# Optimization experiments

Measured on AMD Instinct MI355X. Metric: run time of the kernel, lower is better.

The kernel has to match this reference:

```python
import jax, jax.numpy as jnp
import numpy as np

N, E, C_IN, HID, K, NLAYERS = 1024, 2048, 4, 192, 5, 4


def setup_inputs() -> dict:
    key = jax.random.key(0)
    ks = jax.random.split(key, 24)
    s = 0.05
    x = jax.random.normal(ks[0], (N, C_IN), jnp.float32)
    src = jax.random.randint(ks[1], (E,), 0, N, dtype=jnp.int32)
    off = jax.random.randint(ks[2], (E,), 1, N, dtype=jnp.int32)
    dst = (src + off) % N  # guarantees no self-loops (ChebConv removes them)
    edge_index = jnp.stack([src, dst])  # [2, E] int32
    edge_attr = jax.random.normal(ks[3], (E, C_IN), jnp.float32)
    batch = jnp.zeros((N,), jnp.int32)  # unused by forward, kept for signature fidelity
    inp = {
        'x': x, 'edge_index': edge_index, 'edge_attr': edge_attr, 'batch': batch,
        # ChebConv(4, 192, K=5): K weight mats + bias
        'cheb_w': jax.random.normal(ks[4], (K, C_IN, HID), jnp.float32) * s,
        'cheb_b': jnp.zeros((HID,), jnp.float32),
        # edge encoder Linear(4, 192)
        'eenc_w': jax.random.normal(ks[5], (C_IN, HID), jnp.float32) * s,
        'eenc_b': jnp.zeros((HID,), jnp.float32),
        # 4 NNConv layers, each with MapE2NxN edge MLP (192->192->192*192),
        # root linear (192x192, no bias) and conv bias
        'nn1_w': jax.random.normal(ks[6], (NLAYERS, HID, HID), jnp.float32) * s,
        'nn1_b': jnp.zeros((NLAYERS, HID), jnp.float32),
        'nn2_w': jax.random.normal(ks[7], (NLAYERS, HID, HID * HID), jnp.float32) * (s / 8.0),
        'nn2_b': jnp.zeros((NLAYERS, HID * HID), jnp.float32),
        'root_w': jax.random.normal(ks[8], (NLAYERS, HID, HID), jnp.float32) * s,
        'conv_b': jnp.zeros((NLAYERS, HID), jnp.float32),
        # LayerNorm per DeepGCNLayer
        'ln_g': jnp.ones((NLAYERS, HID), jnp.float32),
        'ln_b': jnp.zeros((NLAYERS, HID), jnp.float32),
        # final Linear(192, 2)
        'out_w': jax.random.normal(ks[9], (HID, 2), jnp.float32) * s,
        'out_b': jnp.zeros((2,), jnp.float32),
    }
    return inp


def _layernorm(v, g, b):
    mu = jnp.mean(v, axis=-1, keepdims=True)
    var = jnp.mean(jnp.square(v - mu), axis=-1, keepdims=True)
    return (v - mu) * jax.lax.rsqrt(var + 1e-5) * g + b


def reference(x, edge_index, edge_attr, batch, cheb_w, cheb_b, eenc_w, eenc_b,
              nn1_w, nn1_b, nn2_w, nn2_b, root_w, conv_b, ln_g, ln_b, out_w, out_b):
    n = x.shape[0]
    src, dst = edge_index[0], edge_index[1]

    # ---- ChebConv (sym norm, lambda_max=2.0) => L_hat = -D^{-1/2} A D^{-1/2} ----
    deg = jax.ops.segment_sum(jnp.ones_like(src, dtype=x.dtype), src, num_segments=n)
    dinv = jnp.where(deg > 0, 1.0 / jnp.sqrt(jnp.maximum(deg, 1.0)), 0.0)
    wnorm = -dinv[src] * dinv[dst]  # [E]

    def lap(v):  # y = L_hat @ v : gather -> weight -> scatter-add
        return jax.ops.segment_sum(wnorm[:, None] * v[src], dst, num_segments=n)

    Tx0 = x
    out = Tx0 @ cheb_w[0]
    Tx1 = lap(Tx0)
    out = out + Tx1 @ cheb_w[1]
    for k in range(2, K):  # Chebyshev recurrence
        Tx2 = 2.0 * lap(Tx1) - Tx0
        out = out + Tx2 @ cheb_w[k]
        Tx0, Tx1 = Tx1, Tx2
    h = out + cheb_b  # [N, HID]

    # ---- edge encoder ----
    ea = edge_attr @ eenc_w + eenc_b  # [E, HID]

    # ---- NNConv: per-edge MLP-generated weight, gather->edge-GEMM->scatter ----
    def nnconv(v, i):
        theta = (ea @ nn1_w[i] + nn1_b[i]) @ nn2_w[i] + nn2_b[i]  # [E, HID*HID]
        theta = theta.reshape(E, HID, HID)
        msg = jnp.einsum('ei,eio->eo', v[src], theta)  # per-edge matvec
        agg = jax.ops.segment_sum(msg, dst, num_segments=n)  # aggr='add'
        return agg + v @ root_w[i] + conv_b[i]

    # layers[0].conv applied directly (no pre-norm/act)
    h = nnconv(h, 0)
    # layers[1:4] are DeepGCNLayer res+: x + conv(dropout(act(norm(x))))
    for i in range(1, NLAYERS):
        z = jax.nn.relu(_layernorm(h, ln_g[i], ln_b[i]))
        h = h + nnconv(z, i)
    # final: act(layers[0].norm(x)), dropout (eval=identity), linear
    h = jax.nn.relu(_layernorm(h, ln_g[0], ln_b[0]))
    return h @ out_w + out_b  # [N, 2]
```

## Files before the change

kernel.cpp:

```cpp
#include <hip/hip_runtime.h>
#include <stdint.h>

typedef _Float16 half8 __attribute__((ext_vector_type(8)));
typedef float f32x4 __attribute__((ext_vector_type(4)));

__global__ __launch_bounds__(256)
void k_pb(const float* __restrict__ nn2_w, const float* __restrict__ eenc_w,
          const float* __restrict__ eenc_b, const float* __restrict__ nn1_w,
          const float* __restrict__ nn1_b, float* __restrict__ Ppart,
          const float* __restrict__ x, const int* __restrict__ ei,
          float* __restrict__ Tx, int* __restrict__ rowptr, int* __restrict__ eord) {
  __shared__ __align__(16) float smem[8192];
  int t = threadIdx.x;
  if (blockIdx.x == 144) {
    if (blockIdx.y == 0 && blockIdx.z == 0) {
      float* cur = smem;
      float* yv = smem + 4096;
      float* deg = yv;
      for (int i = t; i < 1024; i += 256) deg[i] = 0.f;
      __syncthreads();
      for (int e = t; e < 2048; e += 256) atomicAdd(&deg[ei[e]], 1.f);
      __syncthreads();
      float wn[8];
#pragma unroll
      for (int i = 0; i < 8; ++i) {
        int e = t + 256 * i;
        int s = ei[e], d = ei[2048 + e];
        float ds = deg[s], dd = deg[d];
        float a = ds > 0.f ? 1.f / sqrtf(fmaxf(ds, 1.f)) : 0.f;
        float b = dd > 0.f ? 1.f / sqrtf(fmaxf(dd, 1.f)) : 0.f;
        wn[i] = -a * b;
      }
      __syncthreads();
      float4 prev[4];
#pragma unroll
      for (int q = 0; q < 4; ++q) {
        int i = t + 256 * q;
        float4 xv = ((const float4*)x)[i];
        ((float4*)cur)[i] = xv;
        ((float4*)Tx)[i] = xv;
      }
      __syncthreads();
      for (int rec = 0; rec < 4; ++rec) {
        for (int i = t; i < 4096; i += 256) yv[i] = 0.f;
        __syncthreads();
#pragma unroll
        for (int i = 0; i < 8; ++i) {
          int e = t + 256 * i;
          int s = ei[e], d = ei[2048 + e];
          float wv = wn[i];
#pragma unroll
          for (int c = 0; c < 4; ++c) atomicAdd(&yv[d * 4 + c], wv * cur[s * 4 + c]);
        }
        __syncthreads();
        float a = rec ? 2.f : 1.f;
#pragma unroll
        for (int q = 0; q < 4; ++q) {
          int i = t + 256 * q;
          float4 y4 = ((float4*)yv)[i];
          float4 c4 = ((float4*)cur)[i];
          float4 n4;
          n4.x = a * y4.x - (rec ? prev[q].x : 0.f);
          n4.y = a * y4.y - (rec ? prev[q].y : 0.f);
          n4.z = a * y4.z - (rec ? prev[q].z : 0.f);
          n4.w = a * y4.w - (rec ? prev[q].w : 0.f);
          prev[q] = c4;
          ((float4*)cur)[i] = n4;
          ((float4*)(Tx + (rec + 1) * 4096))[i] = n4;
        }
        __syncthreads();
      }
    } else if (blockIdx.y == 1 && blockIdx.z == 0) {
      int* cnt = (int*)smem;
      int* rp  = (int*)smem + 1024;
      int* wtot = (int*)smem + 2048;
      int lane = t & 63, wv = t >> 6;
      for (int i = t; i < 1024; i += 256) cnt[i] = 0;
      __syncthreads();
      for (int e = t; e < 2048; e += 256) atomicAdd(&cnt[ei[2048 + e]], 1);
      __syncthreads();
      int c0 = cnt[t * 4], c1 = cnt[t * 4 + 1], c2 = cnt[t * 4 + 2], c3 = cnt[t * 4 + 3];
      int s = c0 + c1 + c2 + c3;
      int inc = s;
#pragma unroll
      for (int off = 1; off < 64; off <<= 1) {
        int u = __shfl_up(inc, off);
        if (lane >= off) inc += u;
      }
      if (lane == 63) wtot[wv] = inc;
      __syncthreads();
      int woff = 0;
#pragma unroll
      for (int j = 0; j < 4; ++j) if (j < wv) woff += wtot[j];
      int excl = woff + inc - s;
      int4 r4; r4.x = excl; r4.y = excl + c0; r4.z = excl + c0 + c1; r4.w = excl + c0 + c1 + c2;
      *(int4*)(rowptr + t * 4) = r4;
      if (t == 0) rowptr[1024] = 2048;
      rp[t * 4] = r4.x; rp[t * 4 + 1] = r4.y; rp[t * 4 + 2] = r4.z; rp[t * 4 + 3] = r4.w;
      __syncthreads();
      for (int e = t; e < 2048; e += 256) {
        int d = ei[2048 + e];
        int slot = atomicAdd(&rp[d], 1);
        eord[slot] = e;
      }
    }
    return;
  }
  int l = blockIdx.y, kc = blockIdx.z;
  if (t < 192) {
    float a0 = 0.f, a1 = 0.f, a2 = 0.f, a3 = 0.f, a4 = 0.f;
    const float* nw = nn1_w + (size_t)l * 36864 + t;
    for (int k = 0; k < 192; ++k) {
      float nv = nw[(size_t)k * 192];
      a0 += eenc_w[k] * nv;
      a1 += eenc_w[192 + k] * nv;
      a2 += eenc_w[384 + k] * nv;
      a3 += eenc_w[576 + k] * nv;
      a4 += eenc_b[k] * nv;
    }
    smem[t] = a0; smem[192 + t] = a1; smem[384 + t] = a2; smem[576 + t] = a3;
    smem[768 + t] = a4 + nn1_b[l * 192 + t];
  }
  __syncthreads();
  int col = blockIdx.x * 256 + t;
  const float* Wp = nn2_w + (size_t)l * 7077888 + (size_t)(kc * 96) * 36864 + col;
  const float* Mp = smem + kc * 96;
  float a0 = 0.f, a1 = 0.f, a2 = 0.f, a3 = 0.f, a4 = 0.f;
#pragma unroll 8
  for (int k = 0; k < 96; ++k) {
    float wv = Wp[(size_t)k * 36864];
    a0 += wv * Mp[k];
    a1 += wv * Mp[192 + k];
    a2 += wv * Mp[384 + k];
    a3 += wv * Mp[576 + k];
    a4 += wv * Mp[768 + k];
  }
  float* Pp = Ppart + ((size_t)(kc * 4 + l) * 5) * 36864 + col;
  Pp[0] = a0;
  Pp[36864] = a1;
  Pp[2 * 36864] = a2;
  Pp[3 * 36864] = a3;
  Pp[4 * 36864] = a4;
}

__global__ __launch_bounds__(256)
void k_stage(const float* __restrict__ Ppart, const float* __restrict__ nn2_b,
             const float* __restrict__ root_w, _Float16* __restrict__ Btl,
             const float* __restrict__ Tx, const float* __restrict__ cheb_w,
             const float* __restrict__ cheb_b, _Float16* __restrict__ z0) {
  int t = threadIdx.x;
  if (blockIdx.y < 4) {
    int ck = blockIdx.x, l = blockIdx.y;
    _Float16* out = Btl + (size_t)l * 221184 + ck * 9216;
#pragma unroll
    for (int it = 0; it < 5; ++it) {
      int n = it * 256 + t;
      if (n >= 1152) break;
      union { _Float16 h[8]; uint4 v; } u;
      if (n < 960) {
        int c = n / 192, o = n - c * 192;
        const float* P0 = Ppart + ((size_t)(0 * 4 + l) * 5 + c) * 36864;
        const float* P1 = Ppart + ((size_t)(1 * 4 + l) * 5 + c) * 36864;
#pragma unroll
        for (int j = 0; j < 8; ++j) {
          int io = (ck * 8 + j) * 192 + o;
          float val = P0[io] + P1[io];
          if (c == 4) val += nn2_b[(size_t)l * 36864 + io];
          u.h[j] = (_Float16)val;
        }
      } else {
        int o = n - 960;
#pragma unroll
        for (int j = 0; j < 8; ++j)
          u.h[j] = (_Float16)root_w[(size_t)l * 36864 + (ck * 8 + j) * 192 + o];
      }
      *(uint4*)(out + (size_t)n * 8) = u.v;
    }
  } else {
    for (int i = blockIdx.x * 256 + t; i < 24576; i += 6144) {
      int n = i & 1023, ck = i >> 10;
      float tv[5][4];
#pragma unroll
      for (int k = 0; k < 5; ++k) {
        float4 t4 = ((const float4*)(Tx + k * 4096))[n];
        tv[k][0] = t4.x; tv[k][1] = t4.y; tv[k][2] = t4.z; tv[k][3] = t4.w;
      }
      union { _Float16 h[8]; uint4 v; } u;
#pragma unroll
      for (int j = 0; j < 8; ++j) {
        int o = ck * 8 + j;
        float acc = cheb_b[o];
#pragma unroll
        for (int k = 0; k < 5; ++k)
#pragma unroll
          for (int c = 0; c < 4; ++c)
            acc += tv[k][c] * cheb_w[(k * 4 + c) * 192 + o];
        u.h[j] = (_Float16)acc;
      }
      *(uint4*)(z0 + ((size_t)ck * 1024 + n) * 8) = u.v;
    }
  }
}

__global__ __launch_bounds__(256)
void k_y(const _Float16* __restrict__ z16, const _Float16* __restrict__ Btl,
         float* __restrict__ Y, int layer) {
  int t = threadIdx.x;
  int w = t >> 6, lane = t & 63, l15 = lane & 15, q4 = lane >> 4;
  int e0 = blockIdx.x * 64, cb = blockIdx.y;
  const _Float16* Bt = Btl + (size_t)layer * 221184;
  const _Float16* ap = z16 + (((size_t)q4 * 1024) + e0 + w * 16 + l15) * 8;
  const _Float16* bp = Bt + (((size_t)q4 * 1152) + cb * 192 + l15) * 8;
  f32x4 acc[12] = {};
#pragma unroll
  for (int ks = 0; ks < 6; ++ks) {
    half8 av = *(const half8*)(ap + (size_t)ks * 4 * 1024 * 8);
#pragma unroll
    for (int nt = 0; nt < 12; ++nt) {
      half8 bv = *(const half8*)(bp + (size_t)ks * 4 * 1152 * 8 + nt * 16 * 8);
      acc[nt] = __builtin_amdgcn_mfma_f32_16x16x32_f16(av, bv, acc[nt], 0, 0, 0);
    }
  }
#pragma unroll
  for (int nt = 0; nt < 12; ++nt) {
    int col = cb * 192 + nt * 16 + l15;
#pragma unroll
    for (int r = 0; r < 4; ++r) {
      int row = e0 + w * 16 + q4 * 4 + r;
      Y[(size_t)row * 1152 + col] = acc[nt][r];
    }
  }
}

__global__ __launch_bounds__(256)
void k_gn(const int* __restrict__ ei, const float* __restrict__ eattr,
          const int* __restrict__ rowptr, const int* __restrict__ eord,
          const float* __restrict__ Y, const float* __restrict__ hp,
          const float* __restrict__ cbv, const float* __restrict__ gg,
          const float* __restrict__ bb, float* __restrict__ ho,
          _Float16* __restrict__ zo, const float* __restrict__ out_w,
          const float* __restrict__ out_b, float* __restrict__ outp, int l) {
  int t = threadIdx.x, w = t >> 6, lane = t & 63;
  int n = blockIdx.x * 4 + w;
  int o0 = lane, o1 = lane + 64, o2 = lane + 128;
  float v0 = 0.f, v1 = 0.f, v2 = 0.f;
  int beg = rowptr[n], end = rowptr[n + 1];
  for (int idx = beg; idx < end; ++idx) {
    int e = eord[idx];
    int s = ei[e];
    float4 u = ((const float4*)eattr)[e];
    const float* yr = Y + (size_t)s * 1152;
    v0 += yr[o0] * u.x + yr[192 + o0] * u.y + yr[384 + o0] * u.z + yr[576 + o0] * u.w + yr[768 + o0];
    v1 += yr[o1] * u.x + yr[192 + o1] * u.y + yr[384 + o1] * u.z + yr[576 + o1] * u.w + yr[768 + o1];
    v2 += yr[o2] * u.x + yr[192 + o2] * u.y + yr[384 + o2] * u.z + yr[576 + o2] * u.w + yr[768 + o2];
  }
  const float* yn = Y + (size_t)n * 1152 + 960;
  v0 += yn[o0] + cbv[o0]; v1 += yn[o1] + cbv[o1]; v2 += yn[o2] + cbv[o2];
  if (l > 0) {
    v0 += hp[n * 192 + o0]; v1 += hp[n * 192 + o1]; v2 += hp[n * 192 + o2];
  }
  if (l < 3) {
    ho[n * 192 + o0] = v0; ho[n * 192 + o1] = v1; ho[n * 192 + o2] = v2;
  }
  float s1 = v0 + v1 + v2, s2 = v0 * v0 + v1 * v1 + v2 * v2;
#pragma unroll
  for (int off = 32; off >= 1; off >>= 1) {
    s1 += __shfl_xor(s1, off);
    s2 += __shfl_xor(s2, off);
  }
  float mu = s1 * (1.f / 192.f);
  float var = s2 * (1.f / 192.f) - mu * mu;
  float rcp = rsqrtf(var + 1e-5f);
  float z0v = fmaxf((v0 - mu) * rcp * gg[o0] + bb[o0], 0.f);
  float z1v = fmaxf((v1 - mu) * rcp * gg[o1] + bb[o1], 0.f);
  float z2v = fmaxf((v2 - mu) * rcp * gg[o2] + bb[o2], 0.f);
  if (l < 3) {
    zo[((size_t)(o0 >> 3) * 1024 + n) * 8 + (o0 & 7)] = (_Float16)z0v;
    zo[((size_t)(o1 >> 3) * 1024 + n) * 8 + (o1 & 7)] = (_Float16)z1v;
    zo[((size_t)(o2 >> 3) * 1024 + n) * 8 + (o2 & 7)] = (_Float16)z2v;
  } else {
    float a0 = z0v * out_w[o0 * 2] + z1v * out_w[o1 * 2] + z2v * out_w[o2 * 2];
    float a1 = z0v * out_w[o0 * 2 + 1] + z1v * out_w[o1 * 2 + 1] + z2v * out_w[o2 * 2 + 1];
#pragma unroll
    for (int off = 32; off >= 1; off >>= 1) {
      a0 += __shfl_xor(a0, off);
      a1 += __shfl_xor(a1, off);
    }
    if (lane == 0) {
      outp[n * 2] = a0 + out_b[0];
      outp[n * 2 + 1] = a1 + out_b[1];
    }
  }
}

extern "C" void kernel_launch(void* const* d_in, const int* in_sizes, int n_in,
                              void* d_out, int out_size, void* d_ws, size_t ws_size,
                              hipStream_t stream) {
  const float* x      = (const float*)d_in[0];
  const int*   ei     = (const int*)  d_in[1];
  const float* eattr  = (const float*)d_in[2];
  const float* cheb_w = (const float*)d_in[4];
  const float* cheb_b = (const float*)d_in[5];
  const float* eenc_w = (const float*)d_in[6];
  const float* eenc_b = (const float*)d_in[7];
  const float* nn1_w  = (const float*)d_in[8];
  const float* nn1_b  = (const float*)d_in[9];
  const float* nn2_w  = (const float*)d_in[10];
  const float* nn2_b  = (const float*)d_in[11];
  const float* root_w = (const float*)d_in[12];
  const float* conv_b = (const float*)d_in[13];
  const float* ln_g   = (const float*)d_in[14];
  const float* ln_bb  = (const float*)d_in[15];
  const float* out_w  = (const float*)d_in[16];
  const float* out_b  = (const float*)d_in[17];
  float* outp = (float*)d_out;
  (void)in_sizes; (void)n_in; (void)out_size; (void)ws_size;

  char* p = (char*)d_ws;
  _Float16* Btl = (_Float16*)p; p += (size_t)4 * 221184 * 2;
  float* Ppart  = (float*)p;    p += (size_t)2 * 4 * 5 * 36864 * 4;
  float* Tx     = (float*)p;    p += 5 * 4096 * 4;
  float* Y      = (float*)p;    p += (size_t)1024 * 1152 * 4;
  float* hA     = (float*)p;    p += 196608 * 4;
  float* hB     = (float*)p;    p += 196608 * 4;
  _Float16* z0  = (_Float16*)p; p += 196608 * 2;
  _Float16* zA  = (_Float16*)p; p += 196608 * 2;
  _Float16* zB  = (_Float16*)p; p += 196608 * 2;
  int* rowptr   = (int*)p;      p += 1056 * 4;
  int* eord     = (int*)p;      p += 2048 * 4;

  k_pb<<<dim3(145, 4, 2), 256, 0, stream>>>(nn2_w, eenc_w, eenc_b, nn1_w, nn1_b,
                                            Ppart, x, ei, Tx, rowptr, eord);
  k_stage<<<dim3(24, 5), 256, 0, stream>>>(Ppart, nn2_b, root_w, Btl, Tx,
                                           cheb_w, cheb_b, z0);

  const _Float16* zin[4] = {z0, zA, zB, zA};
  _Float16* zout[4] = {zA, zB, zA, zA};
  float* hout[4] = {hA, hB, hA, hA};
  const float* hres[4] = {hA, hA, hB, hA};
  for (int l = 0; l < 4; ++l) {
    k_y<<<dim3(16, 6), 256, 0, stream>>>(zin[l], Btl, Y, l);
    k_gn<<<256, 256, 0, stream>>>(ei, eattr, rowptr, eord, Y, hres[l],
                                  conv_b + (size_t)l * 192,
                                  ln_g + (size_t)((l == 3) ? 0 : (l + 1)) * 192,
                                  ln_bb + (size_t)((l == 3) ? 0 : (l + 1)) * 192,
                                  hout[l], zout[l], out_w, out_b, outp, l);
  }
}
```

Baseline: 299.6 us.

## Split precompute into separate kernel and double-buffer nn2_w streaming via LDS

Moves the per-layer M computation (eenc through nn1), the Chebyshev recurrence and the CSR build out of k_pb into a small k_pre kernel, so the big nn2_w reduction blocks no longer each recompute M. k_pb now handles 512 columns per block, streams 8-row tiles of nn2_w into LDS with global_load_lds in a double-buffered loop, and gives each thread two columns. The aim is better memory-level parallelism on the roughly 113 MB weight read and removal of redundant M work. The cost is an extra kernel launch and a serial dependency on k_pre, whose single Chebyshev block now runs before k_pb instead of alongside it.

Measured after the change: 321.4 us. 7.3% more time.

```diff
diff --git a/kernel.cpp b/kernel.cpp
--- a/kernel.cpp
+++ b/kernel.cpp
@@ -4,143 +4,189 @@
 typedef _Float16 half8 __attribute__((ext_vector_type(8)));
 typedef float f32x4 __attribute__((ext_vector_type(4)));
 
-__global__ __launch_bounds__(256)
-void k_pb(const float* __restrict__ nn2_w, const float* __restrict__ eenc_w,
-          const float* __restrict__ eenc_b, const float* __restrict__ nn1_w,
-          const float* __restrict__ nn1_b, float* __restrict__ Ppart,
-          const float* __restrict__ x, const int* __restrict__ ei,
-          float* __restrict__ Tx, int* __restrict__ rowptr, int* __restrict__ eord) {
+typedef const __attribute__((address_space(1))) void* gptr_t;
+typedef __attribute__((address_space(3))) void* lptr_t;
+static __device__ __forceinline__ void gll16(const void* g, void* l) {
+  __builtin_amdgcn_global_load_lds((gptr_t)(unsigned long long)g,
+                                   (lptr_t)(unsigned int)(unsigned long long)l,
+                                   16, 0, 0);
+}
+
+__global__ __launch_bounds__(256)
+void k_pre(const float* __restrict__ eenc_w, const float* __restrict__ eenc_b,
+           const float* __restrict__ nn1_w, const float* __restrict__ nn1_b,
+           const float* __restrict__ x, const int* __restrict__ ei,
+           float* __restrict__ Mbuf, float* __restrict__ Tx,
+           int* __restrict__ rowptr, int* __restrict__ eord) {
   __shared__ __align__(16) float smem[8192];
   int t = threadIdx.x;
-  if (blockIdx.x == 144) {
-    if (blockIdx.y == 0 && blockIdx.z == 0) {
-      float* cur = smem;
-      float* yv = smem + 4096;
-      float* deg = yv;
-      for (int i = t; i < 1024; i += 256) deg[i] = 0.f;
+  int b = blockIdx.x;
+  if (b < 4) {
+    int l = b;
+    if (t < 192) {
+      float a0 = 0.f, a1 = 0.f, a2 = 0.f, a3 = 0.f, a4 = 0.f;
+      const float* nw = nn1_w + (size_t)l * 36864 + t;
+      for (int k = 0; k < 192; ++k) {
+        float nv = nw[(size_t)k * 192];
+        a0 += eenc_w[k] * nv;
+        a1 += eenc_w[192 + k] * nv;
+        a2 += eenc_w[384 + k] * nv;
+        a3 += eenc_w[576 + k] * nv;
+        a4 += eenc_b[k] * nv;
+      }
+      float* Ml = Mbuf + l * 960;
+      Ml[t] = a0; Ml[192 + t] = a1; Ml[384 + t] = a2; Ml[576 + t] = a3;
+      Ml[768 + t] = a4 + nn1_b[l * 192 + t];
+    }
+  } else if (b == 4) {
+    float* cur = smem;
+    float* yv = smem + 4096;
+    float* deg = yv;
+    for (int i = t; i < 1024; i += 256) deg[i] = 0.f;
+    __syncthreads();
+    for (int e = t; e < 2048; e += 256) atomicAdd(&deg[ei[e]], 1.f);
+    __syncthreads();
+    float wn[8];
+#pragma unroll
+    for (int i = 0; i < 8; ++i) {
+      int e = t + 256 * i;
+      int s = ei[e], d = ei[2048 + e];
+      float ds = deg[s], dd = deg[d];
+      float a = ds > 0.f ? 1.f / sqrtf(fmaxf(ds, 1.f)) : 0.f;
+      float bb = dd > 0.f ? 1.f / sqrtf(fmaxf(dd, 1.f)) : 0.f;
+      wn[i] = -a * bb;
+    }
+    __syncthreads();
+    float4 prev[4];
+#pragma unroll
+    for (int q = 0; q < 4; ++q) {
+      int i = t + 256 * q;
+      float4 xv = ((const float4*)x)[i];
+      ((float4*)cur)[i] = xv;
+      ((float4*)Tx)[i] = xv;
+    }
+    __syncthreads();
+    for (int rec = 0; rec < 4; ++rec) {
+      for (int i = t; i < 4096; i += 256) yv[i] = 0.f;
       __syncthreads();
-      for (int e = t; e < 2048; e += 256) atomicAdd(&deg[ei[e]], 1.f);
-      __syncthreads();
-      float wn[8];
 #pragma unroll
       for (int i = 0; i < 8; ++i) {
         int e = t + 256 * i;
         int s = ei[e], d = ei[2048 + e];
-        float ds = deg[s], dd = deg[d];
-        float a = ds > 0.f ? 1.f / sqrtf(fmaxf(ds, 1.f)) : 0.f;
-        float b = dd > 0.f ? 1.f / sqrtf(fmaxf(dd, 1.f)) : 0.f;
-        wn[i] = -a * b;
+        float wv = wn[i];
+#pragma unroll
+        for (int c = 0; c < 4; ++c) atomicAdd(&yv[d * 4 + c], wv * cur[s * 4 + c]);
       }
       __syncthreads();
-      float4 prev[4];
+      float a = rec ? 2.f : 1.f;
 #pragma unroll
       for (int q = 0; q < 4; ++q) {
         int i = t + 256 * q;
-        float4 xv = ((const float4*)x)[i];
-        ((float4*)cur)[i] = xv;
-        ((float4*)Tx)[i] = xv;
+        float4 y4 = ((float4*)yv)[i];
+        float4 c4 = ((float4*)cur)[i];
+        float4 n4;
+        n4.x = a * y4.x - (rec ? prev[q].x : 0.f);
+        n4.y = a * y4.y - (rec ? prev[q].y : 0.f);
+        n4.z = a * y4.z - (rec ? prev[q].z : 0.f);
+        n4.w = a * y4.w - (rec ? prev[q].w : 0.f);
+        prev[q] = c4;
+        ((float4*)cur)[i] = n4;
+        ((float4*)(Tx + (rec + 1) * 4096))[i] = n4;
       }
       __syncthreads();
-      for (int rec = 0; rec < 4; ++rec) {
-        for (int i = t; i < 4096; i += 256) yv[i] = 0.f;
-        __syncthreads();
-#pragma unroll
-        for (int i = 0; i < 8; ++i) {
-          int e = t + 256 * i;
-          int s = ei[e], d = ei[2048 + e];
-          float wv = wn[i];
-#pragma unroll
-          for (int c = 0; c < 4; ++c) atomicAdd(&yv[d * 4 + c], wv * cur[s * 4 + c]);
-        }
-        __syncthreads();
-        float a = rec ? 2.f : 1.f;
-#pragma unroll
-        for (int q = 0; q < 4; ++q) {
-          int i = t + 256 * q;
-          float4 y4 = ((float4*)yv)[i];
-          float4 c4 = ((float4*)cur)[i];
-          float4 n4;
-          n4.x = a * y4.x - (rec ? prev[q].x : 0.f);
-          n4.y = a * y4.y - (rec ? prev[q].y : 0.f);
-          n4.z = a * y4.z - (rec ? prev[q].z : 0.f);
-          n4.w = a * y4.w - (rec ? prev[q].w : 0.f);
-          prev[q] = c4;
-          ((float4*)cur)[i] = n4;
-          ((float4*)(Tx + (rec + 1) * 4096))[i] = n4;
-        }
-        __syncthreads();
-      }
-    } else if (blockIdx.y == 1 && blockIdx.z == 0) {
-      int* cnt = (int*)smem;
-      int* rp  = (int*)smem + 1024;
-      int* wtot = (int*)smem + 2048;
-      int lane = t & 63, wv = t >> 6;
-      for (int i = t; i < 1024; i += 256) cnt[i] = 0;
-      __syncthreads();
-      for (int e = t; e < 2048; e += 256) atomicAdd(&cnt[ei[2048 + e]], 1);
-      __syncthreads();
-      int c0 = cnt[t * 4], c1 = cnt[t * 4 + 1], c2 = cnt[t * 4 + 2], c3 = cnt[t * 4 + 3];
-      int s = c0 + c1 + c2 + c3;
-      int inc = s;
-#pragma unroll
-      for (int off = 1; off < 64; off <<= 1) {
-        int u = __shfl_up(inc, off);
-        if (lane >= off) inc += u;
-      }
-      if (lane == 63) wtot[wv] = inc;
-      __syncthreads();
-      int woff = 0;
-#pragma unroll
-      for (int j = 0; j < 4; ++j) if (j < wv) woff += wtot[j];
-      int excl = woff + inc - s;
-      int4 r4; r4.x = excl; r4.y = excl + c0; r4.z = excl + c0 + c1; r4.w = excl + c0 + c1 + c2;
-      *(int4*)(rowptr + t * 4) = r4;
-      if (t == 0) rowptr[1024] = 2048;
-      rp[t * 4] = r4.x; rp[t * 4 + 1] = r4.y; rp[t * 4 + 2] = r4.z; rp[t * 4 + 3] = r4.w;
-      __syncthreads();
-      for (int e = t; e < 2048; e += 256) {
-        int d = ei[2048 + e];
-        int slot = atomicAdd(&rp[d], 1);
-        eord[slot] = e;
-      }
-    }
-    return;
-  }
+    }
+  } else {
+    int* cnt = (int*)smem;
+    int* rp  = (int*)smem + 1024;
+    int* wtot = (int*)smem + 2048;
+    int lane = t & 63, wv = t >> 6;
+    for (int i = t; i < 1024; i += 256) cnt[i] = 0;
+    __syncthreads();
+    for (int e = t; e < 2048; e += 256) atomicAdd(&cnt[ei[2048 + e]], 1);
+    __syncthreads();
+    int c0 = cnt[t * 4], c1 = cnt[t * 4 + 1], c2 = cnt[t * 4 + 2], c3 = cnt[t * 4 + 3];
+    int s = c0 + c1 + c2 + c3;
+    int inc = s;
+#pragma unroll
+    for (int off = 1; off < 64; off <<= 1) {
+      int u = __shfl_up(inc, off);
+      if (lane >= off) inc += u;
+    }
+    if (lane == 63) wtot[wv] = inc;
+    __syncthreads();
+    int woff = 0;
+#pragma unroll
+    for (int j = 0; j < 4; ++j) if (j < wv) woff += wtot[j];
+    int excl = woff + inc - s;
+    int4 r4; r4.x = excl; r4.y = excl + c0; r4.z = excl + c0 + c1; r4.w = excl + c0 + c1 + c2;
+    *(int4*)(rowptr + t * 4) = r4;
+    if (t == 0) rowptr[1024] = 2048;
+    rp[t * 4] = r4.x; rp[t * 4 + 1] = r4.y; rp[t * 4 + 2] = r4.z; rp[t * 4 + 3] = r4.w;
+    __syncthreads();
+    for (int e = t; e < 2048; e += 256) {
+      int d = ei[2048 + e];
+      int slot = atomicAdd(&rp[d], 1);
+      eord[slot] = e;
+    }
+  }
+}
+
+__global__ __launch_bounds__(256)
+void k_pb(const float* __restrict__ nn2_w, const float* __restrict__ Mbuf,
+          float* __restrict__ Ppart) {
+  __shared__ __align__(16) float smem[9152];
+  int t = threadIdx.x;
+  int w = t >> 6, lane = t & 63;
   int l = blockIdx.y, kc = blockIdx.z;
-  if (t < 192) {
-    float a0 = 0.f, a1 = 0.f, a2 = 0.f, a3 = 0.f, a4 = 0.f;
-    const float* nw = nn1_w + (size_t)l * 36864 + t;
-    for (int k = 0; k < 192; ++k) {
-      float nv = nw[(size_t)k * 192];
-      a0 += eenc_w[k] * nv;
-      a1 += eenc_w[192 + k] * nv;
-      a2 += eenc_w[384 + k] * nv;
-      a3 += eenc_w[576 + k] * nv;
-      a4 += eenc_b[k] * nv;
-    }
-    smem[t] = a0; smem[192 + t] = a1; smem[384 + t] = a2; smem[576 + t] = a3;
-    smem[768 + t] = a4 + nn1_b[l * 192 + t];
-  }
+  int col0 = blockIdx.x * 512;
+  for (int i = t; i < 960; i += 256) smem[8192 + i] = Mbuf[l * 960 + i];
+  const float* W2l = nn2_w + (size_t)l * 7077888;
+  int k0 = kc * 96;
+
+#define STAGE(b, tile)                                                          \
+  {                                                                             \
+    const float* rowbase = W2l + (size_t)(k0 + (tile) * 8) * 36864 + col0;      \
+    char* lb = (char*)(smem + (b) * 4096);                                      \
+    _Pragma("unroll")                                                           \
+    for (int j = 0; j < 4; ++j) {                                               \
+      int idx = j * 4 + w;                                                      \
+      int row = idx >> 1, sub = idx & 1;                                        \
+      gll16((const char*)(rowbase + (size_t)row * 36864 + sub * 256) + lane * 16, \
+            lb + row * 2048 + sub * 1024 + lane * 16);                          \
+    }                                                                           \
+  }
+
+  float a[5][2] = {};
+  STAGE(0, 0);
   __syncthreads();
-  int col = blockIdx.x * 256 + t;
-  const float* Wp = nn2_w + (size_t)l * 7077888 + (size_t)(kc * 96) * 36864 + col;
-  const float* Mp = smem + kc * 96;
-  float a0 = 0.f, a1 = 0.f, a2 = 0.f, a3 = 0.f, a4 = 0.f;
-#pragma unroll 8
-  for (int k = 0; k < 96; ++k) {
-    float wv = Wp[(size_t)k * 36864];
-    a0 += wv * Mp[k];
-    a1 += wv * Mp[192 + k];
-    a2 += wv * Mp[384 + k];
-    a3 += wv * Mp[576 + k];
-    a4 += wv * Mp[768 + k];
-  }
-  float* Pp = Ppart + ((size_t)(kc * 4 + l) * 5) * 36864 + col;
-  Pp[0] = a0;
-  Pp[36864] = a1;
-  Pp[2 * 36864] = a2;
-  Pp[3 * 36864] = a3;
-  Pp[4 * 36864] = a4;
+  int buf = 0;
+  for (int tile = 0; tile < 12; ++tile) {
+    if (tile < 11) STAGE(buf ^ 1, tile + 1);
+    const float* wb = smem + buf * 4096;
+    const float* Ml = smem + 8192;
+    int kb = k0 + tile * 8;
+#pragma unroll
+    for (int r = 0; r < 8; ++r) {
+      float w0 = wb[r * 512 + 2 * t];
+      float w1 = wb[r * 512 + 2 * t + 1];
+      int k = kb + r;
+#pragma unroll
+      for (int c = 0; c < 5; ++c) {
+        float m = Ml[c * 192 + k];
+        a[c][0] += m * w0;
+        a[c][1] += m * w1;
+      }
+    }
+    __syncthreads();
+    buf ^= 1;
+  }
+#undef STAGE
+  float* Pp = Ppart + ((size_t)(kc * 4 + l) * 5) * 36864 + col0 + 2 * t;
+#pragma unroll
+  for (int c = 0; c < 5; ++c) {
+    Pp[(size_t)c * 36864] = a[c][0];
+    Pp[(size_t)c * 36864 + 1] = a[c][1];
+  }
 }
 
 __global__ __launch_bounds__(256)
@@ -326,11 +372,13 @@
   _Float16* z0  = (_Float16*)p; p += 196608 * 2;
   _Float16* zA  = (_Float16*)p; p += 196608 * 2;
   _Float16* zB  = (_Float16*)p; p += 196608 * 2;
+  float* Mbuf   = (float*)p;    p += 4 * 960 * 4;
   int* rowptr   = (int*)p;      p += 1056 * 4;
   int* eord     = (int*)p;      p += 2048 * 4;
 
-  k_pb<<<dim3(145, 4, 2), 256, 0, stream>>>(nn2_w, eenc_w, eenc_b, nn1_w, nn1_b,
-                                            Ppart, x, ei, Tx, rowptr, eord);
+  k_pre<<<6, 256, 0, stream>>>(eenc_w, eenc_b, nn1_w, nn1_b, x, ei,
+                               Mbuf, Tx, rowptr, eord);
+  k_pb<<<dim3(72, 4, 2), 256, 0, stream>>>(nn2_w, Mbuf, Ppart);
   k_stage<<<dim3(24, 5), 256, 0, stream>>>(Ppart, nn2_b, root_w, Btl, Tx,
                                            cheb_w, cheb_b, z0);
 
```
